# Optimization experiments

Measured on AMD Instinct MI355X. Metric: run time of the kernel, lower is better.

The kernel has to match this reference:

```python
import jax, jax.numpy as jnp
import numpy as np

M1 = M2 = 16      # spectral modes
CM1 = CM2 = 4     # cft modes = modes // 4
L_SEG = 4
M_CHEB = 8
PAD = 9


def _cft2d(x):
    # x: [B,C,H,W]; H,W divisible by L_SEG, segment length divisible by M_CHEB
    B, C, H, W = x.shape
    hs, ws = H // L_SEG, W // L_SEG
    seg = x.reshape(B, C, L_SEG, hs, L_SEG, ws).transpose(0, 1, 2, 4, 3, 5)
    seg = seg.reshape(B, C, L_SEG * L_SEG, hs * ws)  # row-major segment order (i,j)
    seg = seg / jnp.maximum(jnp.linalg.norm(seg, axis=-1, keepdims=True), 1e-12)
    # torch x[:,:,k::M].mean over k=0..M-1 == reshape (n//M, M), mean over rows
    coeffs = seg.reshape(B, C, L_SEG * L_SEG, (hs * ws) // M_CHEB, M_CHEB).mean(axis=3)
    coeffs = coeffs.reshape(B, C, -1)[:, :, : CM1 * CM2]
    return coeffs.reshape(B, C, CM1, CM2)  # real part; imag part is zero


def _spectral_rc(x, w1, w2, g1w, g1b, g2w, g2b):
    B, C, H, W = x.shape
    xft = jnp.fft.rfft2(x, axes=(-2, -1))
    top = jnp.einsum('bixy,ioxy->boxy', xft[:, :, :M1, :M2], w1)
    bot = jnp.einsum('bixy,ioxy->boxy', xft[:, :, H - M1:, :M2], w2)
    out_ft = jnp.zeros((B, w1.shape[1], H, W // 2 + 1), dtype=xft.dtype)
    out_ft = out_ft.at[:, :, :M1, :M2].set(top)
    out_ft = out_ft.at[:, :, H - M1:, :M2].set(bot)
    x_fno = jnp.fft.irfft2(out_ft, s=(H, W), axes=(-2, -1))
    cr = _cft2d(x)
    # torch.view_as_real interleaves (real, imag) on last axis; imag == 0
    cflat = jnp.stack([cr, jnp.zeros_like(cr)], axis=-1).reshape(B, -1)
    h = jax.nn.gelu(cflat @ g1w.T + g1b, approximate=False)
    corr = h @ g2w.T + g2b  # [B, C_out]
    return x_fno + corr[:, :, None, None]


def _forward(x, sw1r, sw1i, sw2r, sw2i, g1w, g1b, g2w, g2b, cw, cb,
             fc0w, fc0b, fc1w, fc1b, fc2w, fc2b):
    B, S1, S2, _ = x.shape
    gx = jnp.broadcast_to(jnp.linspace(0., 1., S1, dtype=x.dtype)[None, :, None, None], (B, S1, S2, 1))
    gy = jnp.broadcast_to(jnp.linspace(0., 1., S2, dtype=x.dtype)[None, None, :, None], (B, S1, S2, 1))
    h = jnp.concatenate([x, gx, gy], axis=-1) @ fc0w.T + fc0b
    h = h.transpose(0, 3, 1, 2)
    h = jnp.pad(h, ((0, 0), (0, 0), (0, PAD), (0, PAD)))
    for l in range(4):
        w1 = sw1r[l] + 1j * sw1i[l]
        w2 = sw2r[l] + 1j * sw2i[l]
        h1 = _spectral_rc(h, w1, w2, g1w[l], g1b[l], g2w[l], g2b[l])
        h2 = jnp.einsum('bchw,oc->bohw', h, cw[l]) + cb[l][None, :, None, None]
        h = h1 + h2
        if l < 3:
            h = jax.nn.gelu(h, approximate=False)
    h = h[..., :-PAD, :-PAD].transpose(0, 2, 3, 1)
    h = jax.nn.gelu(h @ fc1w.T + fc1b, approximate=False)
    return h @ fc2w.T + fc2b


def setup_inputs():
    key = jax.random.key(0)
    ks = jax.random.split(key, 20)
    B, S, Cin, Cout, Wd = 8, 119, 3, 1, 64
    f32 = jnp.float32
    scale = 1.0 / (Wd * Wd)
    return {
        'x': jax.random.normal(ks[0], (B, S, S, Cin), f32),
        'sw1r': scale * jax.random.uniform(ks[1], (4, Wd, Wd, M1, M2), f32),
        'sw1i': scale * jax.random.uniform(ks[2], (4, Wd, Wd, M1, M2), f32),
        'sw2r': scale * jax.random.uniform(ks[3], (4, Wd, Wd, M1, M2), f32),
        'sw2i': scale * jax.random.uniform(ks[4], (4, Wd, Wd, M1, M2), f32),
        'g1w': 0.02 * jax.random.normal(ks[5], (4, 256, 2048), f32),
        'g1b': 0.02 * jax.random.normal(ks[6], (4, 256), f32),
        'g2w': 0.02 * jax.random.normal(ks[7], (4, Wd, 256), f32),
        'g2b': 0.02 * jax.random.normal(ks[8], (4, Wd), f32),
        'cw': (1.0 / 8.0) * jax.random.normal(ks[9], (4, Wd, Wd), f32),
        'cb': 0.1 * jax.random.normal(ks[10], (4, Wd), f32),
        'fc0w': 0.4 * jax.random.normal(ks[11], (Wd, Cin + 2), f32),
        'fc0b': 0.1 * jax.random.normal(ks[12], (Wd,), f32),
        'fc1w': (1.0 / 8.0) * jax.random.normal(ks[13], (128, Wd), f32),
        'fc1b': 0.1 * jax.random.normal(ks[14], (128,), f32),
        'fc2w': (1.0 / 11.3) * jax.random.normal(ks[15], (Cout, 128), f32),
        'fc2b': 0.1 * jax.random.normal(ks[16], (Cout,), f32),
    }


def reference(x, sw1r, sw1i, sw2r, sw2i, g1w, g1b, g2w, g2b, cw, cb,
              fc0w, fc0b, fc1w, fc1b, fc2w, fc2b):
    return _forward(x, sw1r, sw1i, sw2r, sw2i, g1w, g1b, g2w, g2b, cw, cb,
                    fc0w, fc0b, fc1w, fc1b, fc2w, fc2b)
```

## Files before the change

kernel.cpp:

```cpp
#include <hip/hip_runtime.h>
#include <math.h>

#define NB 8
#define NC 64
#define NH 128
#define NW 128
#define NS 119
#define NPIX 113288

__device__ __forceinline__ float gelu_f(float v) {
    return 0.5f * v * (1.0f + erff(v * 0.70710678118654752f));
}

__global__ void __launch_bounds__(128) k_trig(float2* __restrict__ trig) {
    int t = threadIdx.x;
    double a = (double)t * (3.14159265358979323846 / 64.0);
    trig[t] = make_float2((float)cos(a), (float)sin(a));
}

__global__ void __launch_bounds__(128) k_tab(float2* __restrict__ wd) {
    int idx = blockIdx.x * 128 + threadIdx.x;
    int ky = idx >> 7, w = idx & 127;
    int prod = (ky * w) & 127;
    double a = (double)prod * (3.14159265358979323846 / 64.0);
    wd[idx] = make_float2((float)cos(a), (float)(-sin(a)));
}

__global__ void __launch_bounds__(256) k_tc(const float* __restrict__ fc1w,
                                            const float* __restrict__ cw,
                                            float* __restrict__ fc1wT,
                                            float* __restrict__ cwT) {
    int u = blockIdx.x * 256 + threadIdx.x;
    if (u < 8192) {
        int c = u >> 7, j = u & 127;
        fc1wT[u] = fc1w[j * 64 + c];
    } else {
        int v = u - 8192;
        int l = v >> 12, idx = v & 4095;
        int c = idx >> 6, o = idx & 63;
        cwT[v] = cw[l * 4096 + o * 64 + c];
    }
}

__global__ void __launch_bounds__(256) k_fc0(const float* __restrict__ x,
                                             const float* __restrict__ w,
                                             const float* __restrict__ bia,
                                             float* __restrict__ h) {
    __shared__ float sw[320];
    __shared__ float sb[64];
    int t = threadIdx.x;
    for (int u = t; u < 320; u += 256) sw[u] = w[u];
    if (t < 64) sb[t] = bia[t];
    __syncthreads();
    int p = blockIdx.x * 256 + t;
    int b = p >> 14;
    int rem = p & 16383;
    int r = rem >> 7, wc = rem & 127;
    float v0 = 0.f, v1 = 0.f, v2 = 0.f, gx = 0.f, gy = 0.f;
    bool inside = (r < NS) && (wc < NS);
    if (inside) {
        const float* xp = x + ((size_t)(b * NS + r) * NS + wc) * 3;
        v0 = xp[0]; v1 = xp[1]; v2 = xp[2];
        gx = (float)r * (1.0f / 118.0f);
        gy = (float)wc * (1.0f / 118.0f);
    }
    float* hp = h + (size_t)b * NC * NH * NW + rem;
    for (int c = 0; c < 64; ++c) {
        float val = 0.f;
        if (inside) {
            const float* wr = sw + c * 5;
            val = v0 * wr[0] + v1 * wr[1] + v2 * wr[2] + gx * wr[3] + gy * wr[4] + sb[c];
        }
        hp[c * (NH * NW)] = val;
    }
}

__global__ void __launch_bounds__(256) k_mlp1(const float* __restrict__ cr,
                                              const float* __restrict__ g1w,
                                              const float* __restrict__ g1b,
                                              float* __restrict__ hmid) {
    __shared__ float s_cr[8][1024];
    __shared__ float s_wave[4][8];
    int j = blockIdx.x;
    int t = threadIdx.x;
    {
        float* sp = &s_cr[0][0];
        for (int u = t; u < 8192; u += 256) sp[u] = cr[u];
    }
    const float* wrow = g1w + (size_t)j * 2048;
    int v0 = t * 4;
    float w0 = wrow[2 * v0], w1 = wrow[2 * v0 + 2], w2 = wrow[2 * v0 + 4], w3 = wrow[2 * v0 + 6];
    __syncthreads();
    float acc[8];
#pragma unroll
    for (int b = 0; b < 8; ++b) {
        const float* cp = s_cr[b] + v0;
        acc[b] = cp[0] * w0 + cp[1] * w1 + cp[2] * w2 + cp[3] * w3;
    }
#pragma unroll
    for (int d = 32; d > 0; d >>= 1) {
#pragma unroll
        for (int b = 0; b < 8; ++b) acc[b] += __shfl_down(acc[b], d, 64);
    }
    int wv = t >> 6;
    if ((t & 63) == 0) {
#pragma unroll
        for (int b = 0; b < 8; ++b) s_wave[wv][b] = acc[b];
    }
    __syncthreads();
    if (t < 8) {
        float a = s_wave[0][t] + s_wave[1][t] + s_wave[2][t] + s_wave[3][t] + g1b[j];
        hmid[t * 256 + j] = gelu_f(a);
    }
}

__global__ void __launch_bounds__(256) k_mlp2(const float* __restrict__ hmid,
                                              const float* __restrict__ g2w,
                                              const float* __restrict__ g2b,
                                              float* __restrict__ corr) {
    __shared__ float s_h[2048];
    __shared__ float s_w[256];
    int o = blockIdx.x;
    int t = threadIdx.x;
    s_w[t] = g2w[o * 256 + t];
    for (int u = t; u < 2048; u += 256) s_h[u] = hmid[u];
    __syncthreads();
    int b = t >> 5, k = t & 31;
    const float* hp = s_h + b * 256 + k * 8;
    const float* wp = s_w + k * 8;
    float acc = 0.f;
#pragma unroll
    for (int i = 0; i < 8; ++i) acc += hp[i] * wp[i];
#pragma unroll
    for (int d = 16; d > 0; d >>= 1) acc += __shfl_down(acc, d, 32);
    if (k == 0) corr[b * 64 + o] = acc + g2b[o];
}

__global__ void __launch_bounds__(256) k_dft2(const float* __restrict__ h,
                                              float2* __restrict__ xft,
                                              float* __restrict__ cr,
                                              const float2* __restrict__ wd,
                                              const float2* __restrict__ trig) {
    __shared__ __align__(16) float sx[16][132];
    __shared__ __align__(16) float2 sW[16][134];
    __shared__ float2 sT[128][17];
    __shared__ float2 st[128];
    __shared__ float s_cs[2][16][8];
    __shared__ float s_cq[2][16][8];
    int t = threadIdx.x;
    int bc = blockIdx.x;
    if (t < 128) st[t] = trig[t];
    for (int u = t; u < 2048; u += 256) sW[u >> 7][u & 127] = wd[u];
    const float* src = h + (size_t)bc * 16384;
    int r = t >> 4, ky = t & 15;
    float c0a = 0.f, c1a = 0.f, q0a = 0.f, q1a = 0.f;
    for (int ch = 0; ch < 8; ++ch) {
        __syncthreads();
        for (int u = t; u < 2048; u += 256) sx[u >> 7][u & 127] = src[ch * 2048 + u];
        __syncthreads();
        const float* xr = sx[r];
        const float2* wk = sW[ky];
        float re = 0.f, im = 0.f;
#pragma unroll 8
        for (int w0 = 0; w0 < 128; w0 += 4) {
            float4 x4 = *(const float4*)(xr + w0);
            float4 w01 = *(const float4*)(wk + w0);
            float4 w23 = *(const float4*)(wk + w0 + 2);
            re += x4.x * w01.x; im += x4.x * w01.y;
            re += x4.y * w01.z; im += x4.y * w01.w;
            re += x4.z * w23.x; im += x4.z * w23.y;
            re += x4.w * w23.z; im += x4.w * w23.w;
        }
        sT[ch * 16 + r][ky] = make_float2(re, im);
        if (ch < 2 && t < 128) {
            int rr = t >> 3, k = t & 7;
            const float* row = sx[rr];
#pragma unroll
            for (int g = 0; g < 4; ++g) {
                float a = row[g * 8 + k];       c0a += a;  q0a += a * a;
                float bv = row[32 + g * 8 + k]; c1a += bv; q1a += bv * bv;
            }
            if (ch == 1) {
                s_cs[0][rr][k] = c0a; s_cs[1][rr][k] = c1a;
                s_cq[0][rr][k] = q0a; s_cq[1][rr][k] = q1a;
            }
        }
    }
    __syncthreads();
    int mlo = t >> 4;
    int kxa = mlo, kxb = 112 + mlo;
    float2 sva = st[kxa]; float sca = sva.x, ssa = -sva.y;
    float2 svb = st[kxb]; float scb = svb.x, ssb = -svb.y;
    float rea = 0.f, ima = 0.f, reb = 0.f, imb = 0.f;
    for (int h0 = 0; h0 < 128; h0 += 16) {
        float2 bva = st[(kxa * h0) & 127]; float cca = bva.x, csa = -bva.y;
        float2 bvb = st[(kxb * h0) & 127]; float ccb = bvb.x, csb = -bvb.y;
#pragma unroll
        for (int j = 0; j < 16; ++j) {
            float2 Tv = sT[h0 + j][ky];
            rea += Tv.x * cca - Tv.y * csa;
            ima += Tv.x * csa + Tv.y * cca;
            reb += Tv.x * ccb - Tv.y * csb;
            imb += Tv.x * csb + Tv.y * ccb;
            float na = cca * sca - csa * ssa; csa = cca * ssa + csa * sca; cca = na;
            float nb = ccb * scb - csb * ssb; csb = ccb * ssb + csb * scb; ccb = nb;
        }
    }
    float2* xp = xft + (size_t)bc * 512;
    xp[mlo * 16 + ky] = make_float2(rea, ima);
    xp[(mlo + 16) * 16 + ky] = make_float2(reb, imb);
    if (t < 16) {
        int half = t >> 3, k = t & 7;
        float s = 0.f, q = 0.f;
#pragma unroll
        for (int rr = 0; rr < 16; ++rr) s += s_cs[half][rr][k];
        for (int rr = 0; rr < 16; ++rr)
#pragma unroll
            for (int kk = 0; kk < 8; ++kk) q += s_cq[half][rr][kk];
        float norm = fmaxf(sqrtf(q), 1e-12f);
        cr[bc * 16 + t] = s / (128.0f * norm);
    }
}

__global__ void __launch_bounds__(512) k_mix(const float2* __restrict__ xft,
                                             const float* __restrict__ w1r,
                                             const float* __restrict__ w1i,
                                             const float* __restrict__ w2r,
                                             const float* __restrict__ w2i,
                                             float2* __restrict__ F) {
    int rbid = blockIdx.x;
    int m = (rbid & 7) + 8 * ((rbid >> 3) & 3);
    int e = rbid >> 5;
    __shared__ float2 s_w[64][64];
    __shared__ float2 s_x[8][64];
    int t = threadIdx.x;
    const float* wr; const float* wi; int mm;
    if (m < 16) { wr = w1r; wi = w1i; mm = m; } else { wr = w2r; wi = w2i; mm = m - 16; }
    int off = mm * 16 + e;
    for (int u = t; u < 4096; u += 512) {
        s_w[u >> 6][u & 63] = make_float2(wr[(u << 8) + off], wi[(u << 8) + off]);
    }
    {
        int bb = t >> 6, i = t & 63;
        s_x[bb][i] = xft[((size_t)(bb * 64 + i) * 32 + m) * 16 + e];
    }
    __syncthreads();
    int bb = t >> 6, o = t & 63;
    float re = 0.f, im = 0.f;
#pragma unroll 8
    for (int i = 0; i < 64; ++i) {
        float2 xv = s_x[bb][i];
        float2 wv = s_w[i][o];
        re += xv.x * wv.x - xv.y * wv.y;
        im += xv.x * wv.y + xv.y * wv.x;
    }
    F[((size_t)(bb * 16 + e) * 32 + m) * 64 + o] = make_float2(re, im);
}

__global__ void __launch_bounds__(256, 4) k_invb(const float2* __restrict__ F,
                                                 const float* __restrict__ hin,
                                                 const float* __restrict__ cwTl,
                                                 const float* __restrict__ cbl,
                                                 const float* __restrict__ corr,
                                                 const float2* __restrict__ trig,
                                                 float* __restrict__ hout,
                                                 int do_gelu) {
    int blk = blockIdx.x;
    int b = blk >> 7, h = blk & 127;
    __shared__ __align__(16) float s_cwT[64][64];
    __shared__ __align__(16) float2 s_g[16][64];
    __shared__ float2 s_t[128];
    __shared__ float s_co[64];
    int t = threadIdx.x;
    if (t < 128) s_t[t] = trig[t];
    if (t < 64) s_co[t] = corr[b * 64 + t] + cbl[t];
    {
        float* cw0 = &s_cwT[0][0];
        for (int u = t; u < 4096; u += 256) cw0[u] = cwTl[u];
    }
    {
        float2 rot = trig[h];
        int o = t & 63, ky0 = t >> 6;
        const float2* Fb = F + (size_t)b * 32768 + o;
        float a0r=0.f,a0i=0.f,a1r=0.f,a1i=0.f,a2r=0.f,a2i=0.f,a3r=0.f,a3i=0.f;
        float zr = 1.f, zi = 0.f;
        for (int m = 0; m < 16; ++m) {
            const float2* fm = Fb + m * 64;
            float2 f0 = fm[(ky0     ) * 2048];
            float2 f1 = fm[(ky0 +  4) * 2048];
            float2 f2 = fm[(ky0 +  8) * 2048];
            float2 f3 = fm[(ky0 + 12) * 2048];
            a0r += f0.x*zr - f0.y*zi; a0i += f0.x*zi + f0.y*zr;
            a1r += f1.x*zr - f1.y*zi; a1i += f1.x*zi + f1.y*zr;
            a2r += f2.x*zr - f2.y*zi; a2i += f2.x*zi + f2.y*zr;
            a3r += f3.x*zr - f3.y*zi; a3i += f3.x*zi + f3.y*zr;
            float nz = zr*rot.x - zi*rot.y; zi = zr*rot.y + zi*rot.x; zr = nz;
        }
        float z2r = zr, z2i = -zi;
        for (int m = 16; m < 32; ++m) {
            const float2* fm = Fb + m * 64;
            float2 f0 = fm[(ky0     ) * 2048];
            float2 f1 = fm[(ky0 +  4) * 2048];
            float2 f2 = fm[(ky0 +  8) * 2048];
            float2 f3 = fm[(ky0 + 12) * 2048];
            a0r += f0.x*z2r - f0.y*z2i; a0i += f0.x*z2i + f0.y*z2r;
            a1r += f1.x*z2r - f1.y*z2i; a1i += f1.x*z2i + f1.y*z2r;
            a2r += f2.x*z2r - f2.y*z2i; a2i += f2.x*z2i + f2.y*z2r;
            a3r += f3.x*z2r - f3.y*z2i; a3i += f3.x*z2i + f3.y*z2r;
            float nz = z2r*rot.x - z2i*rot.y; z2i = z2r*rot.y + z2i*rot.x; z2r = nz;
        }
        s_g[ky0     ][o] = make_float2(a0r, a0i);
        s_g[ky0 +  4][o] = make_float2(a1r, a1i);
        s_g[ky0 +  8][o] = make_float2(a2r, a2i);
        s_g[ky0 + 12][o] = make_float2(a3r, a3i);
    }
    __syncthreads();
    int ot2 = t >> 6;
    int wt6 = t & 63;
    int o0 = ot2 * 16;
    float acc[16][2];
#pragma unroll
    for (int i = 0; i < 16; ++i) { acc[i][0] = 0.f; acc[i][1] = 0.f; }
    float2 rw0 = s_t[wt6];
    float2 rw1 = s_t[wt6 + 64];
    float z0r = 1.f, z0i = 0.f, z1r = 1.f, z1i = 0.f;
    for (int ky = 0; ky < 16; ++ky) {
        float fs = (ky == 0) ? 1.f : 2.f;
        float tc0 = fs * z0r, ts0 = fs * z0i;
        float tc1 = fs * z1r, ts1 = fs * z1i;
        const float4* gk = (const float4*)(&s_g[ky][o0]);
#pragma unroll
        for (int i2 = 0; i2 < 8; ++i2) {
            float4 g2 = gk[i2];
            acc[2*i2][0]   += g2.x * tc0 - g2.y * ts0;
            acc[2*i2][1]   += g2.x * tc1 - g2.y * ts1;
            acc[2*i2+1][0] += g2.z * tc0 - g2.w * ts0;
            acc[2*i2+1][1] += g2.z * tc1 - g2.w * ts1;
        }
        float nz0 = z0r * rw0.x - z0i * rw0.y; z0i = z0r * rw0.y + z0i * rw0.x; z0r = nz0;
        float nz1 = z1r * rw1.x - z1i * rw1.y; z1i = z1r * rw1.y + z1i * rw1.x; z1r = nz1;
    }
    const float invn = 1.0f / 16384.0f;
#pragma unroll
    for (int i = 0; i < 16; ++i) { acc[i][0] *= invn; acc[i][1] *= invn; }
    const float* hp = hin + ((size_t)(b * 64) * 128 + h) * 128;
    for (int cc = 0; cc < 64; cc += 4) {
        float hv0[4], hv1[4];
#pragma unroll
        for (int c = 0; c < 4; ++c) {
            hv0[c] = hp[(size_t)(cc + c) * 16384 + wt6];
            hv1[c] = hp[(size_t)(cc + c) * 16384 + wt6 + 64];
        }
#pragma unroll
        for (int c = 0; c < 4; ++c) {
            const float4* cwp = (const float4*)(&s_cwT[cc + c][o0]);
#pragma unroll
            for (int i4 = 0; i4 < 4; ++i4) {
                float4 cv = cwp[i4];
                acc[4*i4][0]   += cv.x * hv0[c]; acc[4*i4][1]   += cv.x * hv1[c];
                acc[4*i4+1][0] += cv.y * hv0[c]; acc[4*i4+1][1] += cv.y * hv1[c];
                acc[4*i4+2][0] += cv.z * hv0[c]; acc[4*i4+2][1] += cv.z * hv1[c];
                acc[4*i4+3][0] += cv.w * hv0[c]; acc[4*i4+3][1] += cv.w * hv1[c];
            }
        }
    }
#pragma unroll
    for (int i = 0; i < 16; ++i) {
        int o = o0 + i;
        float co = s_co[o];
        float* outp = hout + ((size_t)(b * 64 + o) * 128 + h) * 128;
        float v0 = acc[i][0] + co;
        float v1 = acc[i][1] + co;
        if (do_gelu) { v0 = gelu_f(v0); v1 = gelu_f(v1); }
        outp[wt6] = v0;
        outp[wt6 + 64] = v1;
    }
}

__global__ void __launch_bounds__(256, 2) k_invbh(const float2* __restrict__ F,
                                                  const float* __restrict__ hin,
                                                  const float* __restrict__ cwTl,
                                                  const float* __restrict__ cbl,
                                                  const float* __restrict__ corr,
                                                  const float2* __restrict__ trig,
                                                  const float* __restrict__ fc1wT,
                                                  const float* __restrict__ fc1b,
                                                  const float* __restrict__ fc2w,
                                                  const float* __restrict__ fc2b,
                                                  float* __restrict__ out) {
    int blk = blockIdx.x;
    int b = blk / 119;
    int h = blk - b * 119;
    __shared__ __align__(16) char smem[32768];
    float*  s_cwT = (float*)smem;
    float2* s_g   = (float2*)(smem + 16384);
    float*  s_hall= (float*)smem;
    __shared__ __align__(16) float s_w8[16][128];
    __shared__ float2 s_t[128];
    __shared__ float s_co[64];
    __shared__ float s_b1[128];
    __shared__ float s_w2[128];
    __shared__ float s_red[4][132];
    int t = threadIdx.x;
    if (t < 128) s_t[t] = trig[t];
    else { s_b1[t - 128] = fc1b[t - 128]; s_w2[t - 128] = fc2w[t - 128]; }
    if (t < 64) s_co[t] = corr[b * 64 + t] + cbl[t];
    for (int u = t; u < 4096; u += 256) s_cwT[u] = cwTl[u];
    {
        float2 rot = trig[h];
        int o = t & 63, ky0 = t >> 6;
        const float2* Fb = F + (size_t)b * 32768 + o;
        float a0r=0.f,a0i=0.f,a1r=0.f,a1i=0.f,a2r=0.f,a2i=0.f,a3r=0.f,a3i=0.f;
        float zr = 1.f, zi = 0.f;
        for (int m = 0; m < 16; ++m) {
            const float2* fm = Fb + m * 64;
            float2 f0 = fm[(ky0     ) * 2048];
            float2 f1 = fm[(ky0 +  4) * 2048];
            float2 f2 = fm[(ky0 +  8) * 2048];
            float2 f3 = fm[(ky0 + 12) * 2048];
            a0r += f0.x*zr - f0.y*zi; a0i += f0.x*zi + f0.y*zr;
            a1r += f1.x*zr - f1.y*zi; a1i += f1.x*zi + f1.y*zr;
            a2r += f2.x*zr - f2.y*zi; a2i += f2.x*zi + f2.y*zr;
            a3r += f3.x*zr - f3.y*zi; a3i += f3.x*zi + f3.y*zr;
            float nz = zr*rot.x - zi*rot.y; zi = zr*rot.y + zi*rot.x; zr = nz;
        }
        float z2r = zr, z2i = -zi;
        for (int m = 16; m < 32; ++m) {
            const float2* fm = Fb + m * 64;
            float2 f0 = fm[(ky0     ) * 2048];
            float2 f1 = fm[(ky0 +  4) * 2048];
            float2 f2 = fm[(ky0 +  8) * 2048];
            float2 f3 = fm[(ky0 + 12) * 2048];
            a0r += f0.x*z2r - f0.y*z2i; a0i += f0.x*z2i + f0.y*z2r;
            a1r += f1.x*z2r - f1.y*z2i; a1i += f1.x*z2i + f1.y*z2r;
            a2r += f2.x*z2r - f2.y*z2i; a2i += f2.x*z2i + f2.y*z2r;
            a3r += f3.x*z2r - f3.y*z2i; a3i += f3.x*z2i + f3.y*z2r;
            float nz = z2r*rot.x - z2i*rot.y; z2i = z2r*rot.y + z2i*rot.x; z2r = nz;
        }
        float2* sg = (float2*)(smem + 16384);
        sg[(ky0     ) * 64 + o] = make_float2(a0r, a0i);
        sg[(ky0 +  4) * 64 + o] = make_float2(a1r, a1i);
        sg[(ky0 +  8) * 64 + o] = make_float2(a2r, a2i);
        sg[(ky0 + 12) * 64 + o] = make_float2(a3r, a3i);
    }
    __syncthreads();
    int ot2 = t >> 6;
    int wt6 = t & 63;
    int o0 = ot2 * 16;
    float acc[16][2];
#pragma unroll
    for (int i = 0; i < 16; ++i) { acc[i][0] = 0.f; acc[i][1] = 0.f; }
    float2 rw0 = s_t[wt6];
    float2 rw1 = s_t[wt6 + 64];
    float z0r = 1.f, z0i = 0.f, z1r = 1.f, z1i = 0.f;
    for (int ky = 0; ky < 16; ++ky) {
        float fs = (ky == 0) ? 1.f : 2.f;
        float tc0 = fs * z0r, ts0 = fs * z0i;
        float tc1 = fs * z1r, ts1 = fs * z1i;
        const float4* gk = (const float4*)(s_g + ky * 64 + o0);
#pragma unroll
        for (int i2 = 0; i2 < 8; ++i2) {
            float4 g2 = gk[i2];
            acc[2*i2][0]   += g2.x * tc0 - g2.y * ts0;
            acc[2*i2][1]   += g2.x * tc1 - g2.y * ts1;
            acc[2*i2+1][0] += g2.z * tc0 - g2.w * ts0;
            acc[2*i2+1][1] += g2.z * tc1 - g2.w * ts1;
        }
        float nz0 = z0r * rw0.x - z0i * rw0.y; z0i = z0r * rw0.y + z0i * rw0.x; z0r = nz0;
        float nz1 = z1r * rw1.x - z1i * rw1.y; z1i = z1r * rw1.y + z1i * rw1.x; z1r = nz1;
    }
    const float invn = 1.0f / 16384.0f;
#pragma unroll
    for (int i = 0; i < 16; ++i) { acc[i][0] *= invn; acc[i][1] *= invn; }
    const float* hp = hin + ((size_t)(b * 64) * 128 + h) * 128;
    for (int cc = 0; cc < 64; cc += 8) {
        float hv0[8], hv1[8];
#pragma unroll
        for (int c = 0; c < 8; ++c) {
            hv0[c] = hp[(size_t)(cc + c) * 16384 + wt6];
            hv1[c] = hp[(size_t)(cc + c) * 16384 + wt6 + 64];
        }
#pragma unroll
        for (int c = 0; c < 8; ++c) {
            const float4* cwp = (const float4*)(s_cwT + (cc + c) * 64 + o0);
#pragma unroll
            for (int i4 = 0; i4 < 4; ++i4) {
                float4 cv = cwp[i4];
                acc[4*i4][0]   += cv.x * hv0[c]; acc[4*i4][1]   += cv.x * hv1[c];
                acc[4*i4+1][0] += cv.y * hv0[c]; acc[4*i4+1][1] += cv.y * hv1[c];
                acc[4*i4+2][0] += cv.z * hv0[c]; acc[4*i4+2][1] += cv.z * hv1[c];
                acc[4*i4+3][0] += cv.w * hv0[c]; acc[4*i4+3][1] += cv.w * hv1[c];
            }
        }
    }
    __syncthreads();
#pragma unroll
    for (int i = 0; i < 16; ++i) {
        float co = s_co[o0 + i];
        s_hall[(o0 + i) * 128 + wt6]      = acc[i][0] + co;
        s_hall[(o0 + i) * 128 + wt6 + 64] = acc[i][1] + co;
    }
    int j0 = ot2 * 32;
    float a32[32][2];
#pragma unroll
    for (int i = 0; i < 32; ++i) { a32[i][0] = 0.f; a32[i][1] = 0.f; }
    for (int cc = 0; cc < 64; cc += 16) {
        __syncthreads();
        for (int u = t; u < 2048; u += 256)
            s_w8[u >> 7][u & 127] = fc1wT[(cc + (u >> 7)) * 128 + (u & 127)];
        __syncthreads();
        for (int c = 0; c < 16; ++c) {
            float hv0 = s_hall[(cc + c) * 128 + wt6];
            float hv1 = s_hall[(cc + c) * 128 + wt6 + 64];
            const float4* wp = (const float4*)(&s_w8[c][j0]);
#pragma unroll
            for (int q = 0; q < 8; ++q) {
                float4 wx = wp[q];
                a32[4*q][0]   += wx.x * hv0; a32[4*q][1]   += wx.x * hv1;
                a32[4*q+1][0] += wx.y * hv0; a32[4*q+1][1] += wx.y * hv1;
                a32[4*q+2][0] += wx.z * hv0; a32[4*q+2][1] += wx.z * hv1;
                a32[4*q+3][0] += wx.w * hv0; a32[4*q+3][1] += wx.w * hv1;
            }
        }
    }
    float sum0 = 0.f, sum1 = 0.f;
#pragma unroll
    for (int i = 0; i < 32; ++i) {
        float b1 = s_b1[j0 + i];
        float w2 = s_w2[j0 + i];
        sum0 += gelu_f(a32[i][0] + b1) * w2;
        sum1 += gelu_f(a32[i][1] + b1) * w2;
    }
    s_red[ot2][wt6] = sum0;
    s_red[ot2][wt6 + 64] = sum1;
    __syncthreads();
    if (t < NS) {
        out[b * (NS * NS) + h * NS + t] =
            fc2b[0] + s_red[0][t] + s_red[1][t] + s_red[2][t] + s_red[3][t];
    }
}

extern "C" void kernel_launch(void* const* d_in, const int* in_sizes, int n_in,
                              void* d_out, int out_size, void* d_ws, size_t ws_size,
                              hipStream_t stream) {
    const float* x    = (const float*)d_in[0];
    const float* sw1r = (const float*)d_in[1];
    const float* sw1i = (const float*)d_in[2];
    const float* sw2r = (const float*)d_in[3];
    const float* sw2i = (const float*)d_in[4];
    const float* g1w  = (const float*)d_in[5];
    const float* g1b  = (const float*)d_in[6];
    const float* g2w  = (const float*)d_in[7];
    const float* g2b  = (const float*)d_in[8];
    const float* cw   = (const float*)d_in[9];
    const float* cb   = (const float*)d_in[10];
    const float* fc0w = (const float*)d_in[11];
    const float* fc0b = (const float*)d_in[12];
    const float* fc1w = (const float*)d_in[13];
    const float* fc1b = (const float*)d_in[14];
    const float* fc2w = (const float*)d_in[15];
    const float* fc2b = (const float*)d_in[16];
    float* out = (float*)d_out;

    char* ws = (char*)d_ws;
    const size_t SZ_H   = (size_t)NB * NC * NH * NW * 4;
    const size_t SZ_XFT = (size_t)NB * NC * 32 * 16 * 8;
    const size_t SZ_F   = SZ_XFT;
    size_t off = 0;
    float2* trig = (float2*)(ws + off); off += 1024;
    float2* wdft = (float2*)(ws + off); off += 2048 * 8;
    float*  f1T  = (float*)(ws + off);  off += 8192 * 4;
    float*  cwT  = (float*)(ws + off);  off += 16384 * 4;
    float*  hA   = (float*)(ws + off);  off += SZ_H;
    float*  hB   = (float*)(ws + off);  off += SZ_H;
    float2* xft  = (float2*)(ws + off); off += SZ_XFT;
    float2* F    = (float2*)(ws + off); off += SZ_F;
    float*  cr   = (float*)(ws + off);  off += (size_t)NB * NC * 16 * 4;
    float*  hmid = (float*)(ws + off);  off += (size_t)NB * 256 * 4;
    float*  corr = (float*)(ws + off);  off += (size_t)NB * 64 * 4;
    (void)ws_size; (void)in_sizes; (void)n_in; (void)out_size;

    k_trig<<<1, 128, 0, stream>>>(trig);
    k_tab<<<16, 128, 0, stream>>>(wdft);
    k_tc<<<96, 256, 0, stream>>>(fc1w, cw, f1T, cwT);
    k_fc0<<<512, 256, 0, stream>>>(x, fc0w, fc0b, hA);

    float* hcur = hA;
    float* hnxt = hB;
    for (int l = 0; l < 4; ++l) {
        const float* w1r = sw1r + (size_t)l * 1048576;
        const float* w1i = sw1i + (size_t)l * 1048576;
        const float* w2r = sw2r + (size_t)l * 1048576;
        const float* w2i = sw2i + (size_t)l * 1048576;
        const float* g1w_l = g1w + (size_t)l * 524288;
        const float* g1b_l = g1b + l * 256;
        const float* g2w_l = g2w + (size_t)l * 16384;
        const float* g2b_l = g2b + l * 64;
        const float* cwT_l = cwT + (size_t)l * 4096;
        const float* cb_l  = cb + l * 64;

        k_dft2<<<512, 256, 0, stream>>>(hcur, xft, cr, wdft, trig);
        k_mlp1<<<256, 256, 0, stream>>>(cr, g1w_l, g1b_l, hmid);
        k_mlp2<<<64, 256, 0, stream>>>(hmid, g2w_l, g2b_l, corr);
        k_mix<<<512, 512, 0, stream>>>(xft, w1r, w1i, w2r, w2i, F);
        if (l < 3) {
            k_invb<<<1024, 256, 0, stream>>>(F, hcur, cwT_l, cb_l, corr, trig, hnxt, 1);
            float* tmp = hcur; hcur = hnxt; hnxt = tmp;
        } else {
            k_invbh<<<NB * NS, 256, 0, stream>>>(F, hcur, cwT_l, cb_l, corr, trig,
                                                 f1T, fc1b, fc2w, fc2b, out);
        }
    }
}
```

Baseline: 510.8 us.

## Fuse gating MLP into mix and inverse kernels, process two rows per DFT thread

Merges the first gating MLP layer into the spectral-mix kernel as extra blocks, and recomputes the second MLP layer inside each inverse-transform block, removing two kernel launches per layer. The row DFT now handles two rows per thread over four 32-row chunks, reusing each twiddle load and halving the sync count. The 1/N scaling is folded into the per-ky factor. In exchange, every inverse block redundantly computes a 64x256 dot product and reads g2w, and the DFT kernel uses more shared memory.

```diff
diff --git a/kernel.cpp b/kernel.cpp
--- a/kernel.cpp
+++ b/kernel.cpp
@@ -75,115 +75,59 @@
     }
 }
 
-__global__ void __launch_bounds__(256) k_mlp1(const float* __restrict__ cr,
-                                              const float* __restrict__ g1w,
-                                              const float* __restrict__ g1b,
-                                              float* __restrict__ hmid) {
-    __shared__ float s_cr[8][1024];
-    __shared__ float s_wave[4][8];
-    int j = blockIdx.x;
-    int t = threadIdx.x;
-    {
-        float* sp = &s_cr[0][0];
-        for (int u = t; u < 8192; u += 256) sp[u] = cr[u];
-    }
-    const float* wrow = g1w + (size_t)j * 2048;
-    int v0 = t * 4;
-    float w0 = wrow[2 * v0], w1 = wrow[2 * v0 + 2], w2 = wrow[2 * v0 + 4], w3 = wrow[2 * v0 + 6];
-    __syncthreads();
-    float acc[8];
-#pragma unroll
-    for (int b = 0; b < 8; ++b) {
-        const float* cp = s_cr[b] + v0;
-        acc[b] = cp[0] * w0 + cp[1] * w1 + cp[2] * w2 + cp[3] * w3;
-    }
-#pragma unroll
-    for (int d = 32; d > 0; d >>= 1) {
-#pragma unroll
-        for (int b = 0; b < 8; ++b) acc[b] += __shfl_down(acc[b], d, 64);
-    }
-    int wv = t >> 6;
-    if ((t & 63) == 0) {
-#pragma unroll
-        for (int b = 0; b < 8; ++b) s_wave[wv][b] = acc[b];
-    }
-    __syncthreads();
-    if (t < 8) {
-        float a = s_wave[0][t] + s_wave[1][t] + s_wave[2][t] + s_wave[3][t] + g1b[j];
-        hmid[t * 256 + j] = gelu_f(a);
-    }
-}
-
-__global__ void __launch_bounds__(256) k_mlp2(const float* __restrict__ hmid,
-                                              const float* __restrict__ g2w,
-                                              const float* __restrict__ g2b,
-                                              float* __restrict__ corr) {
-    __shared__ float s_h[2048];
-    __shared__ float s_w[256];
-    int o = blockIdx.x;
-    int t = threadIdx.x;
-    s_w[t] = g2w[o * 256 + t];
-    for (int u = t; u < 2048; u += 256) s_h[u] = hmid[u];
-    __syncthreads();
-    int b = t >> 5, k = t & 31;
-    const float* hp = s_h + b * 256 + k * 8;
-    const float* wp = s_w + k * 8;
-    float acc = 0.f;
-#pragma unroll
-    for (int i = 0; i < 8; ++i) acc += hp[i] * wp[i];
-#pragma unroll
-    for (int d = 16; d > 0; d >>= 1) acc += __shfl_down(acc, d, 32);
-    if (k == 0) corr[b * 64 + o] = acc + g2b[o];
-}
-
 __global__ void __launch_bounds__(256) k_dft2(const float* __restrict__ h,
                                               float2* __restrict__ xft,
                                               float* __restrict__ cr,
                                               const float2* __restrict__ wd,
                                               const float2* __restrict__ trig) {
-    __shared__ __align__(16) float sx[16][132];
+    __shared__ __align__(16) float sx[32][132];
     __shared__ __align__(16) float2 sW[16][134];
     __shared__ float2 sT[128][17];
     __shared__ float2 st[128];
-    __shared__ float s_cs[2][16][8];
-    __shared__ float s_cq[2][16][8];
+    __shared__ float s_cs[2][32][8];
+    __shared__ float s_cq[2][32][8];
     int t = threadIdx.x;
     int bc = blockIdx.x;
     if (t < 128) st[t] = trig[t];
     for (int u = t; u < 2048; u += 256) sW[u >> 7][u & 127] = wd[u];
     const float* src = h + (size_t)bc * 16384;
-    int r = t >> 4, ky = t & 15;
-    float c0a = 0.f, c1a = 0.f, q0a = 0.f, q1a = 0.f;
-    for (int ch = 0; ch < 8; ++ch) {
+    int rp = t >> 4, ky = t & 15;
+    for (int it = 0; it < 4; ++it) {
         __syncthreads();
-        for (int u = t; u < 2048; u += 256) sx[u >> 7][u & 127] = src[ch * 2048 + u];
+        for (int u = t; u < 4096; u += 256) sx[u >> 7][u & 127] = src[it * 4096 + u];
         __syncthreads();
-        const float* xr = sx[r];
+        const float* xa = sx[2 * rp];
+        const float* xb = sx[2 * rp + 1];
         const float2* wk = sW[ky];
-        float re = 0.f, im = 0.f;
+        float rea = 0.f, ima = 0.f, reb = 0.f, imb = 0.f;
 #pragma unroll 8
         for (int w0 = 0; w0 < 128; w0 += 4) {
-            float4 x4 = *(const float4*)(xr + w0);
+            float4 a4 = *(const float4*)(xa + w0);
+            float4 b4 = *(const float4*)(xb + w0);
             float4 w01 = *(const float4*)(wk + w0);
             float4 w23 = *(const float4*)(wk + w0 + 2);
-            re += x4.x * w01.x; im += x4.x * w01.y;
-            re += x4.y * w01.z; im += x4.y * w01.w;
-            re += x4.z * w23.x; im += x4.z * w23.y;
-            re += x4.w * w23.z; im += x4.w * w23.w;
-        }
-        sT[ch * 16 + r][ky] = make_float2(re, im);
-        if (ch < 2 && t < 128) {
+            rea += a4.x * w01.x; ima += a4.x * w01.y;
+            reb += b4.x * w01.x; imb += b4.x * w01.y;
+            rea += a4.y * w01.z; ima += a4.y * w01.w;
+            reb += b4.y * w01.z; imb += b4.y * w01.w;
+            rea += a4.z * w23.x; ima += a4.z * w23.y;
+            reb += b4.z * w23.x; imb += b4.z * w23.y;
+            rea += a4.w * w23.z; ima += a4.w * w23.w;
+            reb += b4.w * w23.z; imb += b4.w * w23.w;
+        }
+        sT[it * 32 + 2 * rp][ky] = make_float2(rea, ima);
+        sT[it * 32 + 2 * rp + 1][ky] = make_float2(reb, imb);
+        if (it == 0) {
             int rr = t >> 3, k = t & 7;
             const float* row = sx[rr];
+            float cs0 = 0.f, cq0 = 0.f, cs1 = 0.f, cq1 = 0.f;
 #pragma unroll
             for (int g = 0; g < 4; ++g) {
-                float a = row[g * 8 + k];       c0a += a;  q0a += a * a;
-                float bv = row[32 + g * 8 + k]; c1a += bv; q1a += bv * bv;
+                float a = row[g * 8 + k];       cs0 += a;  cq0 += a * a;
+                float bv = row[32 + g * 8 + k]; cs1 += bv; cq1 += bv * bv;
             }
-            if (ch == 1) {
-                s_cs[0][rr][k] = c0a; s_cs[1][rr][k] = c1a;
-                s_cq[0][rr][k] = q0a; s_cq[1][rr][k] = q1a;
-            }
+            s_cs[0][rr][k] = cs0; s_cs[1][rr][k] = cs1;
+            s_cq[0][rr][k] = cq0; s_cq[1][rr][k] = cq1;
         }
     }
     __syncthreads();
@@ -212,56 +156,95 @@
     if (t < 16) {
         int half = t >> 3, k = t & 7;
         float s = 0.f, q = 0.f;
-#pragma unroll
-        for (int rr = 0; rr < 16; ++rr) s += s_cs[half][rr][k];
-        for (int rr = 0; rr < 16; ++rr)
+        for (int rr = 0; rr < 32; ++rr) {
+            s += s_cs[half][rr][k];
 #pragma unroll
             for (int kk = 0; kk < 8; ++kk) q += s_cq[half][rr][kk];
+        }
         float norm = fmaxf(sqrtf(q), 1e-12f);
         cr[bc * 16 + t] = s / (128.0f * norm);
     }
 }
 
-__global__ void __launch_bounds__(512) k_mix(const float2* __restrict__ xft,
-                                             const float* __restrict__ w1r,
-                                             const float* __restrict__ w1i,
-                                             const float* __restrict__ w2r,
-                                             const float* __restrict__ w2i,
-                                             float2* __restrict__ F) {
-    int rbid = blockIdx.x;
-    int m = (rbid & 7) + 8 * ((rbid >> 3) & 3);
-    int e = rbid >> 5;
-    __shared__ float2 s_w[64][64];
-    __shared__ float2 s_x[8][64];
+__global__ void __launch_bounds__(512) k_mixmlp(const float2* __restrict__ xft,
+                                                const float* __restrict__ w1r,
+                                                const float* __restrict__ w1i,
+                                                const float* __restrict__ w2r,
+                                                const float* __restrict__ w2i,
+                                                const float* __restrict__ cr,
+                                                const float* __restrict__ g1w,
+                                                const float* __restrict__ g1b,
+                                                float* __restrict__ hmid,
+                                                float2* __restrict__ F) {
+    __shared__ __align__(16) char smem[36864];
     int t = threadIdx.x;
-    const float* wr; const float* wi; int mm;
-    if (m < 16) { wr = w1r; wi = w1i; mm = m; } else { wr = w2r; wi = w2i; mm = m - 16; }
-    int off = mm * 16 + e;
-    for (int u = t; u < 4096; u += 512) {
-        s_w[u >> 6][u & 63] = make_float2(wr[(u << 8) + off], wi[(u << 8) + off]);
-    }
-    {
-        int bb = t >> 6, i = t & 63;
-        s_x[bb][i] = xft[((size_t)(bb * 64 + i) * 32 + m) * 16 + e];
-    }
-    __syncthreads();
-    int bb = t >> 6, o = t & 63;
-    float re = 0.f, im = 0.f;
+    int bid = blockIdx.x;
+    if (bid < 512) {
+        float2* s_w = (float2*)smem;
+        float2* s_x = (float2*)(smem + 32768);
+        int m = (bid & 7) + 8 * ((bid >> 3) & 3);
+        int e = bid >> 5;
+        const float* wr; const float* wi; int mm;
+        if (m < 16) { wr = w1r; wi = w1i; mm = m; } else { wr = w2r; wi = w2i; mm = m - 16; }
+        int off = mm * 16 + e;
+        for (int u = t; u < 4096; u += 512) {
+            s_w[u] = make_float2(wr[(u << 8) + off], wi[(u << 8) + off]);
+        }
+        {
+            int bb = t >> 6, i = t & 63;
+            s_x[bb * 64 + i] = xft[((size_t)(bb * 64 + i) * 32 + m) * 16 + e];
+        }
+        __syncthreads();
+        int bb = t >> 6, o = t & 63;
+        float re = 0.f, im = 0.f;
 #pragma unroll 8
-    for (int i = 0; i < 64; ++i) {
-        float2 xv = s_x[bb][i];
-        float2 wv = s_w[i][o];
-        re += xv.x * wv.x - xv.y * wv.y;
-        im += xv.x * wv.y + xv.y * wv.x;
-    }
-    F[((size_t)(bb * 16 + e) * 32 + m) * 64 + o] = make_float2(re, im);
+        for (int i = 0; i < 64; ++i) {
+            float2 xv = s_x[bb * 64 + i];
+            float2 wv = s_w[i * 64 + o];
+            re += xv.x * wv.x - xv.y * wv.y;
+            im += xv.x * wv.y + xv.y * wv.x;
+        }
+        F[((size_t)(bb * 16 + e) * 32 + m) * 64 + o] = make_float2(re, im);
+    } else {
+        float* s_cr   = (float*)smem;
+        float* s_wave = (float*)(smem + 32768);
+        int j = bid - 512;
+        for (int u = t; u < 8192; u += 512) s_cr[u] = cr[u];
+        const float* wrow = g1w + (size_t)j * 2048;
+        float w0 = wrow[4 * t], w1 = wrow[4 * t + 2];
+        __syncthreads();
+        float acc[8];
+#pragma unroll
+        for (int b = 0; b < 8; ++b) {
+            float2 v = *(const float2*)(s_cr + b * 1024 + 2 * t);
+            acc[b] = v.x * w0 + v.y * w1;
+        }
+#pragma unroll
+        for (int d = 32; d > 0; d >>= 1) {
+#pragma unroll
+            for (int b = 0; b < 8; ++b) acc[b] += __shfl_down(acc[b], d, 64);
+        }
+        int wv = t >> 6;
+        if ((t & 63) == 0) {
+#pragma unroll
+            for (int b = 0; b < 8; ++b) s_wave[wv * 8 + b] = acc[b];
+        }
+        __syncthreads();
+        if (t < 8) {
+            float a = g1b[j];
+            for (int q = 0; q < 8; ++q) a += s_wave[q * 8 + t];
+            hmid[t * 256 + j] = gelu_f(a);
+        }
+    }
 }
 
 __global__ void __launch_bounds__(256, 4) k_invb(const float2* __restrict__ F,
                                                  const float* __restrict__ hin,
                                                  const float* __restrict__ cwTl,
                                                  const float* __restrict__ cbl,
-                                                 const float* __restrict__ corr,
+                                                 const float* __restrict__ hmid,
+                                                 const float* __restrict__ g2w,
+                                                 const float* __restrict__ g2b,
                                                  const float2* __restrict__ trig,
                                                  float* __restrict__ hout,
                                                  int do_gelu) {
@@ -271,12 +254,21 @@
     __shared__ __align__(16) float2 s_g[16][64];
     __shared__ float2 s_t[128];
     __shared__ float s_co[64];
+    __shared__ float s_part[4][64];
     int t = threadIdx.x;
     if (t < 128) s_t[t] = trig[t];
-    if (t < 64) s_co[t] = corr[b * 64 + t] + cbl[t];
     {
         float* cw0 = &s_cwT[0][0];
         for (int u = t; u < 4096; u += 256) cw0[u] = cwTl[u];
+    }
+    {
+        int o = t & 63, q = t >> 6;
+        const float* hv = hmid + b * 256 + q * 64;
+        const float* gw = g2w + o * 256 + q * 64;
+        float a = 0.f;
+#pragma unroll 8
+        for (int v = 0; v < 64; ++v) a += hv[v] * gw[v];
+        s_part[q][o] = a;
     }
     {
         float2 rot = trig[h];
@@ -315,6 +307,9 @@
         s_g[ky0 + 12][o] = make_float2(a3r, a3i);
     }
     __syncthreads();
+    if (t < 64)
+        s_co[t] = s_part[0][t] + s_part[1][t] + s_part[2][t] + s_part[3][t]
+                + g2b[t] + cbl[t];
     int ot2 = t >> 6;
     int wt6 = t & 63;
     int o0 = ot2 * 16;
@@ -324,8 +319,9 @@
     float2 rw0 = s_t[wt6];
     float2 rw1 = s_t[wt6 + 64];
     float z0r = 1.f, z0i = 0.f, z1r = 1.f, z1i = 0.f;
+    const float invn = 1.0f / 16384.0f;
     for (int ky = 0; ky < 16; ++ky) {
-        float fs = (ky == 0) ? 1.f : 2.f;
+        float fs = (ky == 0) ? invn : (2.f * invn);
         float tc0 = fs * z0r, ts0 = fs * z0i;
         float tc1 = fs * z1r, ts1 = fs * z1i;
         const float4* gk = (const float4*)(&s_g[ky][o0]);
@@ -340,9 +336,6 @@
         float nz0 = z0r * rw0.x - z0i * rw0.y; z0i = z0r * rw0.y + z0i * rw0.x; z0r = nz0;
         float nz1 = z1r * rw1.x - z1i * rw1.y; z1i = z1r * rw1.y + z1i * rw1.x; z1r = nz1;
     }
-    const float invn = 1.0f / 16384.0f;
-#pragma unroll
-    for (int i = 0; i < 16; ++i) { acc[i][0] *= invn; acc[i][1] *= invn; }
     const float* hp = hin + ((size_t)(b * 64) * 128 + h) * 128;
     for (int cc = 0; cc < 64; cc += 4) {
         float hv0[4], hv1[4];
@@ -364,6 +357,7 @@
             }
         }
     }
+    __syncthreads();
 #pragma unroll
     for (int i = 0; i < 16; ++i) {
         int o = o0 + i;
@@ -381,7 +375,9 @@
                                                   const float* __restrict__ hin,
                                                   const float* __restrict__ cwTl,
                                                   const float* __restrict__ cbl,
-                                                  const float* __restrict__ corr,
+                                                  const float* __restrict__ hmid,
+                                                  const float* __restrict__ g2w,
+                                                  const float* __restrict__ g2b,
                                                   const float2* __restrict__ trig,
                                                   const float* __restrict__ fc1wT,
                                                   const float* __restrict__ fc1b,
@@ -401,11 +397,20 @@
     __shared__ float s_b1[128];
     __shared__ float s_w2[128];
     __shared__ float s_red[4][132];
+    __shared__ float s_part[4][64];
     int t = threadIdx.x;
     if (t < 128) s_t[t] = trig[t];
     else { s_b1[t - 128] = fc1b[t - 128]; s_w2[t - 128] = fc2w[t - 128]; }
-    if (t < 64) s_co[t] = corr[b * 64 + t] + cbl[t];
     for (int u = t; u < 4096; u += 256) s_cwT[u] = cwTl[u];
+    {
+        int o = t & 63, q = t >> 6;
+        const float* hv = hmid + b * 256 + q * 64;
+        const float* gw = g2w + o * 256 + q * 64;
+        float a = 0.f;
+#pragma unroll 8
+        for (int v = 0; v < 64; ++v) a += hv[v] * gw[v];
+        s_part[q][o] = a;
+    }
     {
         float2 rot = trig[h];
         int o = t & 63, ky0 = t >> 6;
@@ -444,6 +449,9 @@
         sg[(ky0 + 12) * 64 + o] = make_float2(a3r, a3i);
     }
     __syncthreads();
+    if (t < 64)
+        s_co[t] = s_part[0][t] + s_part[1][t] + s_part[2][t] + s_part[3][t]
+                + g2b[t] + cbl[t];
     int ot2 = t >> 6;
     int wt6 = t & 63;
     int o0 = ot2 * 16;
@@ -453,8 +461,9 @@
     float2 rw0 = s_t[wt6];
     float2 rw1 = s_t[wt6 + 64];
     float z0r = 1.f, z0i = 0.f, z1r = 1.f, z1i = 0.f;
+    const float invn = 1.0f / 16384.0f;
     for (int ky = 0; ky < 16; ++ky) {
-        float fs = (ky == 0) ? 1.f : 2.f;
+        float fs = (ky == 0) ? invn : (2.f * invn);
         float tc0 = fs * z0r, ts0 = fs * z0i;
         float tc1 = fs * z1r, ts1 = fs * z1i;
         const float4* gk = (const float4*)(s_g + ky * 64 + o0);
@@ -469,9 +478,6 @@
         float nz0 = z0r * rw0.x - z0i * rw0.y; z0i = z0r * rw0.y + z0i * rw0.x; z0r = nz0;
         float nz1 = z1r * rw1.x - z1i * rw1.y; z1i = z1r * rw1.y + z1i * rw1.x; z1r = nz1;
     }
-    const float invn = 1.0f / 16384.0f;
-#pragma unroll
-    for (int i = 0; i < 16; ++i) { acc[i][0] *= invn; acc[i][1] *= invn; }
     const float* hp = hin + ((size_t)(b * 64) * 128 + h) * 128;
     for (int cc = 0; cc < 64; cc += 8) {
         float hv0[8], hv1[8];
@@ -577,7 +583,6 @@
     float2* F    = (float2*)(ws + off); off += SZ_F;
     float*  cr   = (float*)(ws + off);  off += (size_t)NB * NC * 16 * 4;
     float*  hmid = (float*)(ws + off);  off += (size_t)NB * 256 * 4;
-    float*  corr = (float*)(ws + off);  off += (size_t)NB * 64 * 4;
     (void)ws_size; (void)in_sizes; (void)n_in; (void)out_size;
 
     k_trig<<<1, 128, 0, stream>>>(trig);
@@ -600,14 +605,15 @@
         const float* cb_l  = cb + l * 64;
 
         k_dft2<<<512, 256, 0, stream>>>(hcur, xft, cr, wdft, trig);
-        k_mlp1<<<256, 256, 0, stream>>>(cr, g1w_l, g1b_l, hmid);
-        k_mlp2<<<64, 256, 0, stream>>>(hmid, g2w_l, g2b_l, corr);
-        k_mix<<<512, 512, 0, stream>>>(xft, w1r, w1i, w2r, w2i, F);
+        k_mixmlp<<<768, 512, 0, stream>>>(xft, w1r, w1i, w2r, w2i,
+                                          cr, g1w_l, g1b_l, hmid, F);
         if (l < 3) {
-            k_invb<<<1024, 256, 0, stream>>>(F, hcur, cwT_l, cb_l, corr, trig, hnxt, 1);
+            k_invb<<<1024, 256, 0, stream>>>(F, hcur, cwT_l, cb_l, hmid,
+                                             g2w_l, g2b_l, trig, hnxt, 1);
             float* tmp = hcur; hcur = hnxt; hnxt = tmp;
         } else {
-            k_invbh<<<NB * NS, 256, 0, stream>>>(F, hcur, cwT_l, cb_l, corr, trig,
+            k_invbh<<<NB * NS, 256, 0, stream>>>(F, hcur, cwT_l, cb_l, hmid,
+                                                 g2w_l, g2b_l, trig,
                                                  f1T, fc1b, fc2w, fc2b, out);
         }
     }
```

After: 499.8 us. 1.02x faster.
